# Kernel tuning notes

Measured on AMD Instinct MI355X. Metric: run time of the kernel, lower is better.

Reference implementation:

```python
import jax, jax.numpy as jnp
import numpy as np

B, L, K, H = 512, 512, 103, 512
I = K + 2  # LSTM input = obs(103) + fed-back pos(2)


def setup_inputs() -> dict:
    key = jax.random.key(0)
    ks = jax.random.split(key, 14)
    s = 0.02
    return {
        "x": jax.random.normal(ks[0], (B, L, K), dtype=jnp.float32),
        "pos": jax.random.normal(ks[1], (B, L, 2), dtype=jnp.float32),
        "hidden_state": jnp.zeros((B, H), dtype=jnp.float32),
        "cell_state": jnp.zeros((B, H), dtype=jnp.float32),
        # LSTM params (PyTorch layout: gates ordered i,f,g,o)
        "W_ih": jax.random.normal(ks[2], (4 * H, I), dtype=jnp.float32) * s,
        "W_hh": jax.random.normal(ks[3], (4 * H, H), dtype=jnp.float32) * s,
        "b_ih": jnp.zeros((4 * H,), dtype=jnp.float32),
        "b_hh": jnp.zeros((4 * H,), dtype=jnp.float32),
        # MLP: H -> 64 -> 16 -> 2, all ReLU
        "W1": jax.random.normal(ks[4], (64, H), dtype=jnp.float32) * s,
        "b1": jnp.zeros((64,), dtype=jnp.float32),
        "W2": jax.random.normal(ks[5], (16, 64), dtype=jnp.float32) * s,
        "b2": jnp.zeros((16,), dtype=jnp.float32),
        "W3": jax.random.normal(ks[6], (2, 16), dtype=jnp.float32) * s,
        "b3": jnp.zeros((2,), dtype=jnp.float32),
    }


def reference(x, pos, hidden_state, cell_state, W_ih, W_hh, b_ih, b_hh,
              W1, b1, W2, b2, W3, b3):
    b = b_ih + b_hh

    def step(carry, x_t):
        h, c, ip = carry  # (B,H),(B,H),(B,2)
        inp = jnp.concatenate([x_t, ip], axis=-1)  # (B, I)
        gates = inp @ W_ih.T + h @ W_hh.T + b      # (B, 4H)
        i, f, g, o = jnp.split(gates, 4, axis=-1)
        c = jax.nn.sigmoid(f) * c + jax.nn.sigmoid(i) * jnp.tanh(g)
        h = jax.nn.sigmoid(o) * jnp.tanh(c)
        y = jax.nn.relu(h @ W1.T + b1)
        y = jax.nn.relu(y @ W2.T + b2)
        y = jax.nn.relu(y @ W3.T + b3)  # (B,2) predicted next pos
        return (h, c, y), y

    xs = jnp.swapaxes(x, 0, 1)  # (L,B,K)
    (h, c, _), ys = jax.lax.scan(step, (hidden_state, cell_state, pos[:, 0, :]), xs)
    predicted_pos = jnp.swapaxes(ys, 0, 1)  # (B,L,2)
    return predicted_pos, h, c
```

## Files before the change

### kernel.cpp

```cpp
#include <hip/hip_runtime.h>

#define NB 512
#define NL 512
#define NK 103
#define NH 512
#define NI 105
#define XROW (NL * NK)

typedef _Float16 half8 __attribute__((ext_vector_type(8)));
typedef _Float16 half4 __attribute__((ext_vector_type(4)));
typedef float floatx4 __attribute__((ext_vector_type(4)));

union U16 { half8 h; unsigned long long u[2]; };

#define XB_STR 136
#define B2_STR 136
#define YST_STR 72
#define Y2_STR 16
#define OFF_XB  0
#define OFF_B2  34816
#define OFF_YST 52224
#define OFF_Y2  61440
#define OFF_FR  63488
#define SMEM_BYTES 65280

#define GBUF  524288
#define GTILE 65536

#define SPIN_MAX (1 << 20)

#define A_LOAD(p)  __hip_atomic_load((p),  __ATOMIC_RELAXED, __HIP_MEMORY_SCOPE_AGENT)
#define A_STORE(p, v) __hip_atomic_store((p), (v), __ATOMIC_RELAXED, __HIP_MEMORY_SCOPE_AGENT)


__device__ __forceinline__ float fast_sigmoid(float v) {
  v = fminf(fmaxf(v, -30.f), 30.f);
  return __builtin_amdgcn_rcpf(1.f + __expf(-v));
}
__device__ __forceinline__ float fast_tanh(float v) {
  v = fminf(fmaxf(v, -15.f), 15.f);
  float e = __expf(-2.f * v);
  return (1.f - e) * __builtin_amdgcn_rcpf(1.f + e);
}

__global__ void __launch_bounds__(256, 1)
lstm_persist(const float* __restrict__ x, const float* __restrict__ pos,
             const float* __restrict__ h0, const float* __restrict__ c0,
             const float* __restrict__ Wih, const float* __restrict__ Whh,
             const float* __restrict__ bih, const float* __restrict__ bhh,
             const float* __restrict__ W1, const float* __restrict__ b1,
             const float* __restrict__ W2, const float* __restrict__ b2,
             const float* __restrict__ W3, const float* __restrict__ b3,
             float* __restrict__ out, void* __restrict__ ws)
{
  extern __shared__ char smem[];
  _Float16* B2s = (_Float16*)(smem + OFF_B2);
  _Float16* YST = (_Float16*)(smem + OFF_YST);
  _Float16* Y2  = (_Float16*)(smem + OFF_Y2);
  _Float16* HTX = Y2;
  float* FR  = (float*)(smem + OFF_FR);
  float* b1s = FR;
  float* b2s = FR + 64;
  float* w3s = FR + 80;
  float* b3s = FR + 112;
  float* wy0 = FR + 114;
  float* wy1 = FR + 178;
  float* bgs = FR + 242;
  float* ypres = FR + 306;
  volatile int* abflag = (volatile int*)(FR + 440);

  const int tid = threadIdx.x;
  const int g  = blockIdx.x & 7;
  const int cs = blockIdx.x >> 3;
  const int w  = tid >> 6, l = tid & 63;
  const int c16 = l & 15, q = l >> 4;
  const int rh = w >> 1;
  const int ch = w & 1;

  unsigned* cnt = (unsigned*)ws + (size_t)g * 16;
  char* hbase = (char*)ws + 4096;

  if (tid == 0) *abflag = 0;

  {
    unsigned* xz = (unsigned*)(smem + OFF_XB);
    for (int i = tid; i < 8704; i += 256) xz[i] = 0;
  }
  for (int idx = tid; idx < 64 * 128; idx += 256) {
    int cc = idx >> 7, k = idx & 127;
    int gr = (cc >> 4) * NH + cs * 16 + (cc & 15);
    float v = (k < NK) ? Wih[(size_t)gr * NI + k] : 0.f;
    B2s[cc * B2_STR + k] = (_Float16)v;
  }
  if (tid < 64) {
    int gr = (tid >> 4) * NH + cs * 16 + (tid & 15);
    wy0[tid] = Wih[(size_t)gr * NI + 103];
    wy1[tid] = Wih[(size_t)gr * NI + 104];
    bgs[tid] = bih[gr] + bhh[gr];
    b1s[tid] = b1[tid];
  }
  if (tid < 16) b2s[tid] = b2[tid];
  if (tid < 32) w3s[tid] = W3[tid];
  if (tid < 2)  b3s[tid] = b3[tid];

  {
    const int r = tid >> 2, hb = tid & 3;
    const float* src = h0 + (size_t)(64 * g + r) * NH + cs * 16 + hb * 4;
    union { unsigned long long u; half4 h; } cv;
    cv.h[0] = (_Float16)src[0]; cv.h[1] = (_Float16)src[1];
    cv.h[2] = (_Float16)src[2]; cv.h[3] = (_Float16)src[3];
    char* dst = hbase + (size_t)g * GTILE + (size_t)(cs >> 1) * 4096
              + (size_t)(r >> 4) * 1024 + (size_t)(r & 15) * 64
              + (size_t)((cs & 1) * 2 + (hb >> 1)) * 16 + (size_t)(hb & 1) * 8;
    A_STORE((unsigned long long*)dst, cv.u);
  }

  half8 bfr[4][16];
  #pragma unroll
  for (int ct = 0; ct < 4; ++ct) {
    const int rown = ch ? (ct * 16 + c16) : (ct * NH + cs * 16 + c16);
    const float* rp = (ch ? W1 : Whh) + (size_t)rown * NH;
    #pragma unroll
    for (int kk = 0; kk < 16; ++kk) {
      const float* p = rp + kk * 32 + q * 8;
      floatx4 f0 = *(const floatx4*)(p);
      floatx4 f1 = *(const floatx4*)(p + 4);
      half8 hv;
      hv[0]=(_Float16)f0[0]; hv[1]=(_Float16)f0[1]; hv[2]=(_Float16)f0[2]; hv[3]=(_Float16)f0[3];
      hv[4]=(_Float16)f1[0]; hv[5]=(_Float16)f1[1]; hv[6]=(_Float16)f1[2]; hv[7]=(_Float16)f1[3];
      bfr[ct][kk] = hv;
    }
  }
  half8 w2f[2];
  if (ch) {
    #pragma unroll
    for (int kk = 0; kk < 2; ++kk) {
      const float* p = W2 + c16 * 64 + kk * 32 + q * 8;
      floatx4 f0 = *(const floatx4*)(p);
      floatx4 f1 = *(const floatx4*)(p + 4);
      half8 hv;
      hv[0]=(_Float16)f0[0]; hv[1]=(_Float16)f0[1]; hv[2]=(_Float16)f0[2]; hv[3]=(_Float16)f0[3];
      hv[4]=(_Float16)f1[0]; hv[5]=(_Float16)f1[1]; hv[6]=(_Float16)f1[2]; hv[7]=(_Float16)f1[3];
      w2f[kk] = hv;
    }
  }
  float cacc[2][4];
  if (!ch) {
    #pragma unroll
    for (int rt = 0; rt < 2; ++rt)
      #pragma unroll
      for (int reg = 0; reg < 4; ++reg)
        cacc[rt][reg] = c0[(size_t)(64 * g + 32 * rh + 16 * rt + q * 4 + reg) * NH + cs * 16 + c16];
  }

  auto xstage = [&](int t1) {
    _Float16* xb = (_Float16*)(smem + OFF_XB) + (size_t)(t1 & 1) * 64 * XB_STR;
    const int row = 32 * rh + (l >> 1);
    const int p = l & 1;
    const float* src = x + (size_t)(64 * g + row) * XROW + (size_t)t1 * NK + p * 52;
    _Float16* dst = xb + row * XB_STR + p * 52;
    const int nfull = p ? 12 : 13;
    for (int cnk = 0; cnk < nfull; ++cnk) {
      float f0 = src[cnk * 4 + 0], f1 = src[cnk * 4 + 1];
      float f2 = src[cnk * 4 + 2], f3 = src[cnk * 4 + 3];
      half4 hv; hv[0]=(_Float16)f0; hv[1]=(_Float16)f1; hv[2]=(_Float16)f2; hv[3]=(_Float16)f3;
      *(half4*)(dst + cnk * 4) = hv;
    }
    if (p) {
      dst[48] = (_Float16)src[48];
      dst[49] = (_Float16)src[49];
      dst[50] = (_Float16)src[50];
    }
  };

  __syncthreads();
  if (!ch) xstage(0);
  __syncthreads();
  if (tid == 0)
    __hip_atomic_fetch_add(cnt, 1u, __ATOMIC_RELAXED, __HIP_MEMORY_SCOPE_AGENT);

  for (int t = 0; t <= NL; ++t) {
    {
      const unsigned target = 32u * (unsigned)(t + 1);
      int spins = 0;
      while (A_LOAD(cnt) < target) {
        if (++spins > SPIN_MAX) { *abflag = 1; break; }
      }
    }

    U16 ar[2][16];
    {
      const char* lb = hbase + (size_t)(t & 1) * GBUF + (size_t)g * GTILE
                     + (size_t)(2 * rh) * 1024 + (size_t)c16 * 64 + (size_t)q * 16;
      #pragma unroll
      for (int kk = 0; kk < 16; ++kk) {
        #pragma unroll
        for (int rt = 0; rt < 2; ++rt) {
          const unsigned long long* up =
              (const unsigned long long*)(lb + (size_t)kk * 4096 + rt * 1024);
          ar[rt][kk].u[0] = A_LOAD(up);
          ar[rt][kk].u[1] = A_LOAD(up + 1);
        }
      }
    }

    floatx4 acc[4][2] = {};

    if (!ch && t < NL) {
      const _Float16* xb = (const _Float16*)(smem + OFF_XB) + (size_t)(t & 1) * 64 * XB_STR;
      #pragma unroll
      for (int kb = 0; kb < 4; ++kb) {
        half8 ax[2];
        #pragma unroll
        for (int rt = 0; rt < 2; ++rt)
          ax[rt] = *(const half8*)(xb + (32 * rh + 16 * rt + c16) * XB_STR + kb * 32 + q * 8);
        #pragma unroll
        for (int ct = 0; ct < 4; ++ct) {
          half8 bf = *(const half8*)(B2s + (ct * 16 + c16) * B2_STR + kb * 32 + q * 8);
          #pragma unroll
          for (int rt = 0; rt < 2; ++rt)
            acc[ct][rt] = __builtin_amdgcn_mfma_f32_16x16x32_f16(ax[rt], bf, acc[ct][rt], 0, 0, 0);
        }
      }
      if (t + 1 < NL) xstage(t + 1);
    }

    #pragma unroll
    for (int kk = 0; kk < 16; ++kk)
      #pragma unroll
      for (int ct = 0; ct < 4; ++ct) {
        acc[ct][0] = __builtin_amdgcn_mfma_f32_16x16x32_f16(ar[0][kk].h, bfr[ct][kk], acc[ct][0], 0, 0, 0);
        acc[ct][1] = __builtin_amdgcn_mfma_f32_16x16x32_f16(ar[1][kk].h, bfr[ct][kk], acc[ct][1], 0, 0, 0);
      }

    if (ch) {
      if (t == 0) {
        if (l < 32) {
          int row = 32 * rh + l;
          const float* pp = pos + (size_t)(64 * g + row) * (NL * 2);
          ypres[row * 2 + 0] = pp[0];
          ypres[row * 2 + 1] = pp[1];
        }
      } else {
        #pragma unroll
        for (int ct = 0; ct < 4; ++ct)
          #pragma unroll
          for (int rt = 0; rt < 2; ++rt)
            #pragma unroll
            for (int reg = 0; reg < 4; ++reg) {
              int row = 32 * rh + 16 * rt + q * 4 + reg;
              float v = acc[ct][rt][reg] + b1s[ct * 16 + c16];
              YST[row * YST_STR + ct * 16 + c16] = (_Float16)fmaxf(v, 0.f);
            }
        floatx4 a2c[2] = {};
        #pragma unroll
        for (int kk2 = 0; kk2 < 2; ++kk2)
          #pragma unroll
          for (int rt = 0; rt < 2; ++rt) {
            half8 af = *(const half8*)(YST + (32 * rh + 16 * rt + c16) * YST_STR + kk2 * 32 + q * 8);
            a2c[rt] = __builtin_amdgcn_mfma_f32_16x16x32_f16(af, w2f[kk2], a2c[rt], 0, 0, 0);
          }
        #pragma unroll
        for (int rt = 0; rt < 2; ++rt)
          #pragma unroll
          for (int reg = 0; reg < 4; ++reg) {
            int row = 32 * rh + 16 * rt + q * 4 + reg;
            float v = a2c[rt][reg] + b2s[c16];
            Y2[row * Y2_STR + c16] = (_Float16)fmaxf(v, 0.f);
          }
        if (l < 32) {
          int row = 32 * rh + l;
          float y0 = b3s[0], y1 = b3s[1];
          #pragma unroll
          for (int k = 0; k < 16; ++k) {
            float vv = (float)Y2[row * Y2_STR + k];
            y0 += vv * w3s[k];
            y1 += vv * w3s[16 + k];
          }
          y0 = fmaxf(y0, 0.f); y1 = fmaxf(y1, 0.f);
          ypres[row * 2 + 0] = y0;
          ypres[row * 2 + 1] = y1;
          if (cs == 0) {
            float2* op = (float2*)(out + (size_t)(64 * g + row) * (NL * 2) + (size_t)(t - 1) * 2);
            *op = make_float2(y0, y1);
          }
        }
      }
    }
    __syncthreads();
    if (*abflag) return;

    if (!ch && t < NL) {
      #pragma unroll
      for (int rt = 0; rt < 2; ++rt)
        #pragma unroll
        for (int reg = 0; reg < 4; ++reg) {
          int rl = 32 * rh + 16 * rt + q * 4 + reg;
          float yp0 = ypres[rl * 2], yp1 = ypres[rl * 2 + 1];
          float gi = acc[0][rt][reg] + bgs[c16]      + yp0 * wy0[c16]      + yp1 * wy1[c16];
          float gf = acc[1][rt][reg] + bgs[16 + c16] + yp0 * wy0[16 + c16] + yp1 * wy1[16 + c16];
          float gg = acc[2][rt][reg] + bgs[32 + c16] + yp0 * wy0[32 + c16] + yp1 * wy1[32 + c16];
          float go = acc[3][rt][reg] + bgs[48 + c16] + yp0 * wy0[48 + c16] + yp1 * wy1[48 + c16];
          float iv = fast_sigmoid(gi);
          float fv = fast_sigmoid(gf);
          float gv = fast_tanh(gg);
          float ov = fast_sigmoid(go);
          float cn = fv * cacc[rt][reg] + iv * gv;
          cacc[rt][reg] = cn;
          float hn = ov * fast_tanh(cn);
          HTX[rl * 16 + c16] = (_Float16)hn;
          if (t == NL - 1) {
            out[(size_t)(NB * NL * 2) + (size_t)(64 * g + rl) * NH + cs * 16 + c16] = hn;
            out[(size_t)(NB * NL * 2) + (size_t)(NB * NH) + (size_t)(64 * g + rl) * NH + cs * 16 + c16] = cn;
          }
        }
    }

    if (t < NL) {
      __syncthreads();
      {
        const int r = tid >> 2, hb = tid & 3;
        char* dst = hbase + (size_t)((t + 1) & 1) * GBUF + (size_t)g * GTILE
                  + (size_t)(cs >> 1) * 4096
                  + (size_t)(r >> 4) * 1024 + (size_t)(r & 15) * 64
                  + (size_t)((cs & 1) * 2 + (hb >> 1)) * 16 + (size_t)(hb & 1) * 8;
        unsigned long long v = *(const unsigned long long*)(HTX + r * 16 + hb * 4);
        A_STORE((unsigned long long*)dst, v);
      }
      __syncthreads();
      if (tid == 0)
        __hip_atomic_fetch_add(cnt, 1u, __ATOMIC_RELAXED, __HIP_MEMORY_SCOPE_AGENT);
    }
  }
}

extern "C" void kernel_launch(void* const* d_in, const int* in_sizes, int n_in,
                              void* d_out, int out_size, void* d_ws, size_t ws_size,
                              hipStream_t stream) {
  (void)in_sizes; (void)n_in; (void)out_size; (void)ws_size;
  const float* x   = (const float*)d_in[0];
  const float* pos = (const float*)d_in[1];
  const float* h0  = (const float*)d_in[2];
  const float* c0  = (const float*)d_in[3];
  const float* Wih = (const float*)d_in[4];
  const float* Whh = (const float*)d_in[5];
  const float* bih = (const float*)d_in[6];
  const float* bhh = (const float*)d_in[7];
  const float* W1  = (const float*)d_in[8];
  const float* b1  = (const float*)d_in[9];
  const float* W2  = (const float*)d_in[10];
  const float* b2  = (const float*)d_in[11];
  const float* W3  = (const float*)d_in[12];
  const float* b3  = (const float*)d_in[13];
  float* out = (float*)d_out;

  hipMemsetAsync(d_ws, 0, 4096, stream);

  void* args[] = { (void*)&x, (void*)&pos, (void*)&h0, (void*)&c0,
                   (void*)&Wih, (void*)&Whh, (void*)&bih, (void*)&bhh,
                   (void*)&W1, (void*)&b1, (void*)&W2, (void*)&b2,
                   (void*)&W3, (void*)&b3, (void*)&out, (void*)&d_ws };

  hipError_t err = hipLaunchCooperativeKernel(
      reinterpret_cast<void*>(lstm_persist),
      dim3(256, 1, 1), dim3(256, 1, 1), args, (unsigned)SMEM_BYTES, stream);
  if (err != hipSuccess) {
    (void)hipGetLastError();
    lstm_persist<<<dim3(256, 1, 1), dim3(256, 1, 1), SMEM_BYTES, stream>>>(
        x, pos, h0, c0, Wih, Whh, bih, bhh, W1, b1, W2, b2, W3, b3, out, d_ws);
  }
}
```

Measured before the change: 5.458 ms.

## Replace atomic counter barrier with per-block flags and publish h from registers

```diff
diff --git a/kernel.cpp b/kernel.cpp
--- a/kernel.cpp
+++ b/kernel.cpp
@@ -57,7 +57,6 @@
   _Float16* B2s = (_Float16*)(smem + OFF_B2);
   _Float16* YST = (_Float16*)(smem + OFF_YST);
   _Float16* Y2  = (_Float16*)(smem + OFF_Y2);
-  _Float16* HTX = Y2;
   float* FR  = (float*)(smem + OFF_FR);
   float* b1s = FR;
   float* b2s = FR + 64;
@@ -77,7 +76,7 @@
   const int rh = w >> 1;
   const int ch = w & 1;
 
-  unsigned* cnt = (unsigned*)ws + (size_t)g * 16;
+  unsigned* flags = (unsigned*)ws;
   char* hbase = (char*)ws + 4096;
 
   if (tid == 0) *abflag = 0;
@@ -176,14 +175,16 @@
   __syncthreads();
   if (!ch) xstage(0);
   __syncthreads();
-  if (tid == 0)
-    __hip_atomic_fetch_add(cnt, 1u, __ATOMIC_RELAXED, __HIP_MEMORY_SCOPE_AGENT);
+  if (tid == 0) A_STORE(flags + ((g << 5) + cs) * 4, 1u);
+
+  char* pub0 = hbase + (size_t)g * GTILE + (size_t)(cs >> 1) * 4096
+             + (size_t)((cs & 1) * 2 + (c16 >> 3)) * 16 + (size_t)(c16 & 4) * 2;
 
   for (int t = 0; t <= NL; ++t) {
-    {
-      const unsigned target = 32u * (unsigned)(t + 1);
+    if (l < 32) {
+      const unsigned* f = flags + ((g << 5) + l) * 4;
       int spins = 0;
-      while (A_LOAD(cnt) < target) {
+      while (A_LOAD(f) < (unsigned)(t + 1)) {
         if (++spins > SPIN_MAX) { *abflag = 1; break; }
       }
     }
@@ -291,6 +292,7 @@
     if (*abflag) return;
 
     if (!ch && t < NL) {
+      char* pb = pub0 + (size_t)((t + 1) & 1) * GBUF;
       #pragma unroll
       for (int rt = 0; rt < 2; ++rt)
         #pragma unroll
@@ -308,7 +310,17 @@
           float cn = fv * cacc[rt][reg] + iv * gv;
           cacc[rt][reg] = cn;
           float hn = ov * fast_tanh(cn);
-          HTX[rl * 16 + c16] = (_Float16)hn;
+          union { _Float16 h; unsigned short us; } hc; hc.h = (_Float16)hn;
+          unsigned hu = (unsigned)hc.us;
+          unsigned s1 = __shfl_xor(hu, 1, 64);
+          unsigned packed = (hu & 0xFFFFu) | (s1 << 16);
+          unsigned p2 = __shfl_xor(packed, 2, 64);
+          if ((c16 & 3) == 0) {
+            unsigned long long pv = (unsigned long long)packed
+                                  | ((unsigned long long)p2 << 32);
+            A_STORE((unsigned long long*)(pb + (size_t)(rl >> 4) * 1024
+                                             + (size_t)(rl & 15) * 64), pv);
+          }
           if (t == NL - 1) {
             out[(size_t)(NB * NL * 2) + (size_t)(64 * g + rl) * NH + cs * 16 + c16] = hn;
             out[(size_t)(NB * NL * 2) + (size_t)(NB * NH) + (size_t)(64 * g + rl) * NH + cs * 16 + c16] = cn;
@@ -318,18 +330,7 @@
 
     if (t < NL) {
       __syncthreads();
-      {
-        const int r = tid >> 2, hb = tid & 3;
-        char* dst = hbase + (size_t)((t + 1) & 1) * GBUF + (size_t)g * GTILE
-                  + (size_t)(cs >> 1) * 4096
-                  + (size_t)(r >> 4) * 1024 + (size_t)(r & 15) * 64
-                  + (size_t)((cs & 1) * 2 + (hb >> 1)) * 16 + (size_t)(hb & 1) * 8;
-        unsigned long long v = *(const unsigned long long*)(HTX + r * 16 + hb * 4);
-        A_STORE((unsigned long long*)dst, v);
-      }
-      __syncthreads();
-      if (tid == 0)
-        __hip_atomic_fetch_add(cnt, 1u, __ATOMIC_RELAXED, __HIP_MEMORY_SCOPE_AGENT);
+      if (tid == 0) A_STORE(flags + ((g << 5) + cs) * 4, (unsigned)(t + 2));
     }
   }
 }
```

Result: slower. 6.506 ms (+19.2%).
